# Kernel optimization log

Measured on AMD Instinct MI355X. Metric: run time of the kernel, lower is better.

The kernel has to match this reference:

```python
import jax, jax.numpy as jnp
import numpy as np

N_HEADS = 16
D_K = 64
MAX_LEN = 5000


def setup_inputs() -> dict:
    key = jax.random.key(0)
    ks = jax.random.split(key, 6)
    B, L, D = 4, 1024, 1024
    s = 1.0 / np.sqrt(D).astype(np.float32)
    return {
        "x": jax.random.normal(ks[0], (B, L, D), jnp.float32),
        "W_q": jax.random.normal(ks[1], (D, D), jnp.float32) * s,
        "b_q": jnp.zeros((D,), jnp.float32),
        "W_k": jax.random.normal(ks[2], (D, D), jnp.float32) * s,
        "b_k": jnp.zeros((D,), jnp.float32),
        "W_v": jax.random.normal(ks[3], (D, D), jnp.float32) * s,
        "b_v": jnp.zeros((D,), jnp.float32),
        "W_o": jax.random.normal(ks[4], (D, D), jnp.float32) * s,
        "b_o": jnp.zeros((D,), jnp.float32),
        "Er": jax.random.normal(ks[5], (MAX_LEN, D_K), jnp.float32) * 0.02,
    }


def reference(x, W_q, b_q, W_k, b_k, W_v, b_v, W_o, b_o, Er):
    B, L, D = x.shape
    H = N_HEADS
    dk = D // H
    # torch nn.Linear: y = x @ W.T + b
    Q = (x @ W_q.T + b_q).reshape(B, L, H, dk).transpose(0, 2, 1, 3)  # (B,H,L,dk)
    K = (x @ W_k.T + b_k).reshape(B, L, H, dk).transpose(0, 2, 1, 3)
    V = (x @ W_v.T + b_v).reshape(B, L, H, dk).transpose(0, 2, 1, 3)
    AC = jnp.einsum('bhid,bhjd->bhij', Q, K)  # (B,H,L,L)
    rel_pos = jnp.arange(L - 1, -L, -1) + (MAX_LEN - 1)  # (2L-1,)
    # mode='clip' matches intended math: clamped rows fall in the part that
    # the relative shift slices away.
    Er_embed = jnp.take(Er, rel_pos, axis=0, mode='clip')  # (2L-1, dk)
    BD = jnp.einsum('bhid,rd->bhir', Q, Er_embed)  # (B,H,L,2L-1)
    # _relative_shift: view is a no-op (shape already (B,H,L,2L-1)), then slice
    BD = BD[..., L - 1:]  # (B,H,L,L)
    scores = (AC + BD) / np.sqrt(dk).astype(np.float32)
    attn = jax.nn.softmax(scores, axis=-1)
    out = jnp.einsum('bhij,bhjd->bhid', attn, V)
    out = out.transpose(0, 2, 1, 3).reshape(B, L, D)
    return out @ W_o.T + b_o
```

## Files before the change

kernel.cpp:

```cpp
#include <hip/hip_runtime.h>
#include <cstdint>
#include <cstddef>


typedef __attribute__((ext_vector_type(8))) short short8;
typedef __attribute__((ext_vector_type(4))) float f32x4;

#define MFMA_BF16(a, b, c) __builtin_amdgcn_mfma_f32_16x16x32_bf16((a), (b), (c), 0, 0, 0)

constexpr int kB = 4, kL = 1024, kD = 1024, kH = 16;
constexpr int kBL = kB * kL;
constexpr float kScale = 0.125f * 1.44269504088896340736f;

static __device__ __forceinline__ unsigned short f32_to_bf16(float f) {
  union { float f; uint32_t u; } c; c.f = f;
  uint32_t u = c.u + 0x7fffu + ((c.u >> 16) & 1u);
  return (unsigned short)(u >> 16);
}

static __device__ __forceinline__ uint32_t pack_bf16x2(float a, float b) {
  union { float f; uint32_t u; } ca, cb; ca.f = a; cb.f = b;
  return ((ca.u + 0x8000u) >> 16) | ((cb.u + 0x8000u) & 0xffff0000u);
}

static __device__ __forceinline__ void gload_lds16(const void* g, void* l) {
  __builtin_amdgcn_global_load_lds(
      (const __attribute__((address_space(1))) void*)g,
      (__attribute__((address_space(3))) void*)l, 16, 0, 0);
}

__global__ __launch_bounds__(256)
void cast_all(const float* __restrict__ x,  const float* __restrict__ Wq,
              const float* __restrict__ Wk, const float* __restrict__ Wv,
              const float* __restrict__ Wo,
              unsigned short* __restrict__ xb, unsigned short* __restrict__ Wcat,
              unsigned short* __restrict__ Wob) {
  int i = blockIdx.x * blockDim.x + threadIdx.x;
  const float* src;
  ushort4* dst;
  int off;
  if (i < 1048576) {
    src = x; dst = reinterpret_cast<ushort4*>(xb); off = i;
  } else {
    int j = i - 1048576;
    int seg = j >> 18;
    off = j & 262143;
    if (seg == 0)      { src = Wq; dst = reinterpret_cast<ushort4*>(Wcat); }
    else if (seg == 1) { src = Wk; dst = reinterpret_cast<ushort4*>(Wcat) + 262144; }
    else if (seg == 2) { src = Wv; dst = reinterpret_cast<ushort4*>(Wcat) + 524288; }
    else               { src = Wo; dst = reinterpret_cast<ushort4*>(Wob); }
  }
  float4 v = reinterpret_cast<const float4*>(src)[off];
  ushort4 o;
  o.x = f32_to_bf16(v.x); o.y = f32_to_bf16(v.y);
  o.z = f32_to_bf16(v.z); o.w = f32_to_bf16(v.w);
  dst[off] = o;
}

__global__ __launch_bounds__(512, 2)
void gemm_qkv(const unsigned short* __restrict__ A,
              const unsigned short* __restrict__ Bm,
              const float* __restrict__ bq, const float* __restrict__ bk,
              const float* __restrict__ bv,
              const float* __restrict__ Er,
              unsigned short* __restrict__ Qh, unsigned short* __restrict__ Kh,
              unsigned short* __restrict__ Vth) {
  __shared__ __align__(16) char smem[114688];
  const int tid  = threadIdx.x;
  const int lane = tid & 63, wave = tid >> 6;
  const int quad = lane >> 4, l15 = lane & 15;
  const int wr = wave >> 2, wc = wave & 3;

  const int bid = blockIdx.x;
  const int xcd = bid & 7, idx = bid >> 3;
  const int m0 = ((xcd >> 1) * 4 + (idx >> 3)) * 256;
  const int n0 = ((xcd & 1) * 8 + (idx & 7)) * 192;

  const int aoff = (l15 >> 1) * 128 + (l15 & 1) * 64 +
                   ((quad * 16) ^ (((l15 >> 1) & 3) << 4)) + wr * 8192;
  const int b_lane = (quad * 16) ^ ((l15 & 7) << 4);
  const int boff = (wc * 48 + l15) * 128 + b_lane;

  int srowA[2], scolA[2];
#pragma unroll
  for (int j = 0; j < 2; ++j) {
    int poff = (j * 512 + tid) * 16;
    int L = poff ^ (((poff >> 7) & 3) << 4);
    srowA[j] = ((L >> 7) << 1) | ((L >> 6) & 1);
    scolA[j] = (L & 63) >> 1;
  }
  int srowB[3], scolB[3];
#pragma unroll
  for (int j = 0; j < 3; ++j) {
    int poff = (j * 512 + tid) * 16;
    int L = poff ^ (((poff >> 7) & 7) << 4);
    srowB[j] = L >> 7;
    scolB[j] = (L & 127) >> 1;
  }

  auto stageA = [&](int kh, int tt) {
    char* dst = smem + (tt & 1) * 32768 + kh * 16384 + tid * 16;
    const int kc = tt * 64 + kh * 32;
#pragma unroll
    for (int j = 0; j < 2; ++j)
      gload_lds16(A + (size_t)(m0 + srowA[j]) * 1024 + kc + scolA[j],
                  dst + j * 8192);
  };
  auto stageB = [&](int tt) {
    char* dst = smem + 65536 + (tt & 1) * 24576 + tid * 16;
    const int kc = tt * 64;
#pragma unroll
    for (int j = 0; j < 3; ++j)
      gload_lds16(Bm + (size_t)(n0 + srowB[j]) * 1024 + kc + scolB[j],
                  dst + j * 8192);
  };

  const f32x4 vzero = {0.f, 0.f, 0.f, 0.f};
  f32x4 acc[8][3];
#pragma unroll
  for (int i = 0; i < 8; ++i)
#pragma unroll
    for (int j = 0; j < 3; ++j) acc[i][j] = vzero;

  stageA(0, 0); stageB(0); stageA(1, 0); stageA(0, 1);
  asm volatile("s_waitcnt vmcnt(4)" ::: "memory");
  __builtin_amdgcn_s_barrier();

#define LDA(KH, MB) do {                                                      \
    _Pragma("unroll")                                                         \
    for (int f_ = 0; f_ < 4; ++f_)                                            \
      af[f_] = *(const short8*)(RA + (KH) * 16384 + aoff + ((MB) + f_) * 1024); \
  } while (0)
#define LDB(KH) do {                                                          \
    _Pragma("unroll")                                                         \
    for (int n_ = 0; n_ < 3; ++n_)                                            \
      bf[n_] = *(const short8*)(RB + ((boff + n_ * 2048) ^ ((KH) * 64)));     \
  } while (0)
#define BARA() do {                                                           \
    __builtin_amdgcn_s_barrier();                                             \
    asm volatile("s_waitcnt lgkmcnt(0)" ::: "memory");                        \
    __builtin_amdgcn_sched_barrier(0);                                        \
  } while (0)
#define MFMA_12(MB) do {                                                      \
    __builtin_amdgcn_s_setprio(1);                                            \
    _Pragma("unroll")                                                         \
    for (int mq_ = 0; mq_ < 4; ++mq_) {                                       \
      _Pragma("unroll")                                                       \
      for (int nq_ = 0; nq_ < 3; ++nq_)                                       \
        acc[(MB) + mq_][nq_] =                                                \
            MFMA_BF16(af[mq_], bf[nq_], acc[(MB) + mq_][nq_]);                \
    }                                                                         \
    __builtin_amdgcn_s_setprio(0);                                            \
  } while (0)

  for (int t = 0; t < 16; ++t) {
    const char* RA = smem + (t & 1) * 32768;
    const char* RB = smem + 65536 + (t & 1) * 24576;
    short8 af[4], bf[3];
    LDA(0, 0); LDB(0);
    if (t + 1 < 16) stageB(t + 1);
    BARA(); MFMA_12(0);
    __builtin_amdgcn_s_barrier();
    LDA(0, 4);
    if (t + 1 < 16) stageA(1, t + 1);
    BARA(); MFMA_12(4);
    if (t < 15) asm volatile("s_waitcnt vmcnt(7)" ::: "memory");
    else        asm volatile("s_waitcnt vmcnt(0)" ::: "memory");
    __builtin_amdgcn_s_barrier();
    LDA(1, 0); LDB(1);
    if (t + 2 < 16) stageA(0, t + 2);
    BARA(); MFMA_12(0);
    __builtin_amdgcn_s_barrier();
    LDA(1, 4);
    BARA(); MFMA_12(4);
    if (t < 14)       asm volatile("s_waitcnt vmcnt(4)" ::: "memory");
    else if (t == 14) asm volatile("s_waitcnt vmcnt(2)" ::: "memory");
    else              asm volatile("s_waitcnt vmcnt(0)" ::: "memory");
    __builtin_amdgcn_s_barrier();
  }

#undef LDA
#undef LDB
#undef BARA
#undef MFMA_12

  __syncthreads();
  const int gmb = m0 + wr * 128;
  const int bb  = gmb >> 10, i0l = gmb & 1023;
  unsigned short* Wv = (unsigned short*)smem + (size_t)wave * 6144;

#pragma unroll
  for (int nf = 0; nf < 3; ++nf) {
    const int n    = n0 + wc * 48 + nf * 16;
    const int wsel = n >> 10;
    const int nin  = n & 1023;
    const int hh   = nin >> 6, d0 = nin & 63;
    const size_t bh = (size_t)(bb * 16 + hh);

    if (wsel == 0) {
#pragma unroll
      for (int mf = 0; mf < 8; ++mf)
#pragma unroll
        for (int r = 0; r < 4; ++r) {
          const int i = i0l + mf * 16 + quad * 4 + r;
          float v = (acc[mf][nf][r] + bq[nin + l15]) * kScale;
          Qh[(bh * 1024 + i) * 64 + d0 + l15] = f32_to_bf16(v);
        }
    } else if (wsel == 1) {
#pragma unroll
      for (int mf = 0; mf < 8; ++mf)
#pragma unroll
        for (int r = 0; r < 4; ++r) {
          const int i = i0l + mf * 16 + quad * 4 + r;
          float v = acc[mf][nf][r] + bk[nin + l15] +
                    Er[(size_t)(4999 - i) * 64 + d0 + l15];
          Kh[(bh * 1024 + i) * 64 + d0 + l15] = f32_to_bf16(v);
        }
    } else {
      unsigned short* Wn = Wv + nf * 2048;
#pragma unroll
      for (int mf = 0; mf < 8; ++mf) {
        ushort4 pk;
        pk.x = f32_to_bf16(acc[mf][nf][0] + bv[nin + l15]);
        pk.y = f32_to_bf16(acc[mf][nf][1] + bv[nin + l15]);
        pk.z = f32_to_bf16(acc[mf][nf][2] + bv[nin + l15]);
        pk.w = f32_to_bf16(acc[mf][nf][3] + bv[nin + l15]);
        *(ushort4*)&Wn[(size_t)l15 * 128 + mf * 16 + quad * 4] = pk;
      }
#pragma unroll
      for (int p = 0; p < 4; ++p) {
        const int u = p * 64 + lane;
        const int dl = u >> 4, ch = (u & 15) * 8;
        short8 vv = *(const short8*)&Wn[(size_t)dl * 128 + ch];
        *(short8*)&Vth[(bh * 64 + d0 + dl) * 1024 + i0l + ch] = vv;
      }
    }
  }
}

__global__ __launch_bounds__(256)
void gemm_out(const unsigned short* __restrict__ A,
              const unsigned short* __restrict__ Bm,
              const float* __restrict__ bias,
              float* __restrict__ outf) {
  __shared__ __align__(16) char smem[49152];
  const int tid  = threadIdx.x;
  const int lane = tid & 63, wave = tid >> 6;
  const int quad = lane >> 4, l15 = lane & 15;
  const int m0 = blockIdx.y * 128, n0 = blockIdx.x * 64;

  const int afo = (l15 >> 1) * 128 + (l15 & 1) * 64 +
                  ((quad * 16) ^ (((l15 >> 1) & 3) << 4));

  int arow[4], acol[4], akh[4];
#pragma unroll
  for (int j = 0; j < 4; ++j) {
    int u = j * 256 + tid;
    akh[j] = u >> 9;
    int poff = (u & 511) * 16;
    int L = poff ^ (((poff >> 7) & 3) << 4);
    arow[j] = ((L >> 7) << 1) | ((L >> 6) & 1);
    acol[j] = (L & 63) >> 1;
  }
  int brow[2], bcol[2], bkh[2];
#pragma unroll
  for (int j = 0; j < 2; ++j) {
    int u = j * 256 + tid;
    bkh[j] = u >> 8;
    int poff = (u & 255) * 16;
    int L = poff ^ (((poff >> 7) & 3) << 4);
    brow[j] = ((L >> 7) << 1) | ((L >> 6) & 1);
    bcol[j] = (L & 63) >> 1;
  }

  auto stageG = [&](int buf, int t) {
    char* base = smem + buf * 24576;
    const int kc = t * 64;
#pragma unroll
    for (int j = 0; j < 4; ++j) {
      int u = j * 256 + tid;
      gload_lds16(A + (size_t)(m0 + arow[j]) * 1024 + kc + akh[j] * 32 + acol[j],
                  base + u * 16);
    }
#pragma unroll
    for (int j = 0; j < 2; ++j) {
      int u = j * 256 + tid;
      gload_lds16(Bm + (size_t)(n0 + brow[j]) * 1024 + kc + bkh[j] * 32 + bcol[j],
                  base + 16384 + u * 16);
    }
  };

  const f32x4 vzero = {0.f, 0.f, 0.f, 0.f};
  f32x4 acc[2][4];
#pragma unroll
  for (int i = 0; i < 2; ++i)
#pragma unroll
    for (int j = 0; j < 4; ++j) acc[i][j] = vzero;

  stageG(0, 0);
  for (int t = 0; t < 16; ++t) {
    const int cur = t & 1;
    if (t < 15) stageG(cur ^ 1, t + 1);
    if (t < 15) asm volatile("s_waitcnt vmcnt(6)" ::: "memory");
    else        asm volatile("s_waitcnt vmcnt(0)" ::: "memory");
    __builtin_amdgcn_s_barrier();
    __builtin_amdgcn_sched_barrier(0);
    const char* Ab = smem + cur * 24576;
    const char* Bb = Ab + 16384;
#pragma unroll
    for (int ks = 0; ks < 2; ++ks) {
      short8 af[2], bfv[4];
#pragma unroll
      for (int mt = 0; mt < 2; ++mt)
        af[mt] = *(const short8*)(Ab + ks * 8192 + wave * 2048 + mt * 1024 + afo);
#pragma unroll
      for (int nt = 0; nt < 4; ++nt)
        bfv[nt] = *(const short8*)(Bb + ks * 4096 + nt * 1024 + afo);
#pragma unroll
      for (int mt = 0; mt < 2; ++mt)
#pragma unroll
        for (int nt = 0; nt < 4; ++nt)
          acc[mt][nt] = MFMA_BF16(af[mt], bfv[nt], acc[mt][nt]);
    }
    __builtin_amdgcn_s_barrier();
    __builtin_amdgcn_sched_barrier(0);
  }

#pragma unroll
  for (int mt = 0; mt < 2; ++mt)
#pragma unroll
    for (int nt = 0; nt < 4; ++nt)
#pragma unroll
      for (int r = 0; r < 4; ++r) {
        const int gm = m0 + wave * 32 + mt * 16 + quad * 4 + r;
        const int gn = n0 + nt * 16 + l15;
        outf[(size_t)gm * 1024 + gn] = acc[mt][nt][r] + bias[gn];
      }
}

__global__ __launch_bounds__(256)
void attn_kernel(const unsigned short* __restrict__ Q,
                 const unsigned short* __restrict__ Kp,
                 const unsigned short* __restrict__ Vt,
                 unsigned short* __restrict__ Ao) {
  __shared__ unsigned short Ks[2][2][64 * 32];
  __shared__ unsigned short Vs[2][2][64 * 32];
  __shared__ unsigned short Plds[4][32 * 72];
  const int tid  = threadIdx.x;
  const int lane = tid & 63, wave = tid >> 6;
  const int quad = lane >> 4, l15 = lane & 15;
  const int bh = blockIdx.x;
  const int qb = blockIdx.y;
  const size_t base  = (size_t)bh * (kL * 64);
  const size_t vbase = (size_t)bh * (64 * kL);
  const int i0 = qb * 128 + wave * 32;

  short8 qf[2][2];
#pragma unroll
  for (int mt = 0; mt < 2; ++mt)
#pragma unroll
    for (int ks = 0; ks < 2; ++ks)
      qf[mt][ks] = *(const short8*)
          &Q[base + (size_t)(i0 + mt * 16 + l15) * 64 + ks * 32 + quad * 8];

  auto stage = [&](int buf, int kb) {
#pragma unroll
    for (int j = 0; j < 2; ++j) {
      int u = j * 256 + tid;
      int half = u >> 8, row = (u >> 2) & 63, c = (u & 3) * 8;
      gload_lds16(Kp + base + (size_t)(kb * 64 + row) * 64 + half * 32 + c,
                  (char*)&Ks[buf][0][0] + (size_t)u * 16);
      gload_lds16(Vt + vbase + (size_t)row * kL + kb * 64 + half * 32 + c,
                  (char*)&Vs[buf][0][0] + (size_t)u * 16);
    }
  };

  const f32x4 vzero = {0.f, 0.f, 0.f, 0.f};
  f32x4 of[2][4];
#pragma unroll
  for (int mt = 0; mt < 2; ++mt)
#pragma unroll
    for (int dt = 0; dt < 4; ++dt) of[mt][dt] = vzero;
  float lsum[2] = {0.f, 0.f};

  unsigned short* Pw = Plds[wave];

  stage(0, 0);
  __syncthreads();

  for (int kb = 0; kb < 16; ++kb) {
    const int cur = kb & 1, nxt = cur ^ 1;
    if (kb < 15) stage(nxt, kb + 1);

    short8 kf[4][2];
#pragma unroll
    for (int nt = 0; nt < 4; ++nt)
#pragma unroll
      for (int ks = 0; ks < 2; ++ks)
        kf[nt][ks] = *(const short8*)&Ks[cur][ks][(nt * 16 + l15) * 32 + quad * 8];
    f32x4 sf[2][4];
#pragma unroll
    for (int mt = 0; mt < 2; ++mt)
#pragma unroll
      for (int nt = 0; nt < 4; ++nt) {
        sf[mt][nt] = MFMA_BF16(kf[nt][0], qf[mt][0], vzero);
        sf[mt][nt] = MFMA_BF16(kf[nt][1], qf[mt][1], sf[mt][nt]);
      }

#pragma unroll
    for (int mt = 0; mt < 2; ++mt)
#pragma unroll
      for (int nt = 0; nt < 4; ++nt) {
        float p0 = __builtin_amdgcn_exp2f(sf[mt][nt][0]);
        float p1 = __builtin_amdgcn_exp2f(sf[mt][nt][1]);
        float p2 = __builtin_amdgcn_exp2f(sf[mt][nt][2]);
        float p3 = __builtin_amdgcn_exp2f(sf[mt][nt][3]);
        lsum[mt] += (p0 + p1) + (p2 + p3);
        uint2 w;
        w.x = pack_bf16x2(p0, p1);
        w.y = pack_bf16x2(p2, p3);
        *(uint2*)&Pw[(mt * 16 + l15) * 72 + nt * 16 + quad * 4] = w;
      }
    short8 pf[2][2];
#pragma unroll
    for (int mt = 0; mt < 2; ++mt)
#pragma unroll
      for (int ks = 0; ks < 2; ++ks)
        pf[mt][ks] = *(const short8*)&Pw[(mt * 16 + l15) * 72 + ks * 32 + quad * 8];

    short8 vf[4][2];
#pragma unroll
    for (int dt = 0; dt < 4; ++dt)
#pragma unroll
      for (int ks = 0; ks < 2; ++ks)
        vf[dt][ks] = *(const short8*)&Vs[cur][ks][(dt * 16 + l15) * 32 + quad * 8];
#pragma unroll
    for (int mt = 0; mt < 2; ++mt)
#pragma unroll
      for (int dt = 0; dt < 4; ++dt) {
        of[mt][dt] = MFMA_BF16(pf[mt][0], vf[dt][0], of[mt][dt]);
        of[mt][dt] = MFMA_BF16(pf[mt][1], vf[dt][1], of[mt][dt]);
      }

    __syncthreads();
  }

  float rl[2][4];
#pragma unroll
  for (int mt = 0; mt < 2; ++mt) {
    float s = lsum[mt];
    s += __shfl_xor(s, 16);
    s += __shfl_xor(s, 32);
#pragma unroll
    for (int r = 0; r < 4; ++r)
      rl[mt][r] = __builtin_amdgcn_rcpf(__shfl(s, quad * 4 + r));
  }

  const int b = bh >> 4, h = bh & 15;
#pragma unroll
  for (int mt = 0; mt < 2; ++mt)
#pragma unroll
    for (int dt = 0; dt < 4; ++dt)
#pragma unroll
      for (int r = 0; r < 4; ++r) {
        const int ig = i0 + mt * 16 + quad * 4 + r;
        float v = of[mt][dt][r] * rl[mt][r];
        Ao[((size_t)(b * 1024 + ig)) * 1024 + h * 64 + dt * 16 + l15] = f32_to_bf16(v);
      }
}

extern "C" void kernel_launch(void* const* d_in, const int* in_sizes, int n_in,
                              void* d_out, int out_size, void* d_ws, size_t ws_size,
                              hipStream_t stream) {
  const float* x   = (const float*)d_in[0];
  const float* W_q = (const float*)d_in[1];
  const float* b_q = (const float*)d_in[2];
  const float* W_k = (const float*)d_in[3];
  const float* b_k = (const float*)d_in[4];
  const float* W_v = (const float*)d_in[5];
  const float* b_v = (const float*)d_in[6];
  const float* W_o = (const float*)d_in[7];
  const float* b_o = (const float*)d_in[8];
  const float* Er  = (const float*)d_in[9];
  float* out = (float*)d_out;

  char* ws = (char*)d_ws;
  unsigned short* xb   = (unsigned short*)(ws + (size_t)0);
  unsigned short* Wcat = (unsigned short*)(ws + ((size_t)8  << 20));
  unsigned short* Wob  = (unsigned short*)(ws + ((size_t)14 << 20));
  unsigned short* Qh   = (unsigned short*)(ws + ((size_t)16 << 20));
  unsigned short* Kh   = (unsigned short*)(ws + ((size_t)24 << 20));
  unsigned short* Vth  = (unsigned short*)(ws + ((size_t)32 << 20));
  unsigned short* Aoh  = (unsigned short*)(ws + ((size_t)40 << 20));

  cast_all<<<8192, 256, 0, stream>>>(x, W_q, W_k, W_v, W_o, xb, Wcat, Wob);

  gemm_qkv<<<256, 512, 0, stream>>>(
      xb, Wcat, b_q, b_k, b_v, Er, Qh, Kh, Vth);

  attn_kernel<<<dim3(kB * kH, kL / 128), 256, 0, stream>>>(Qh, Kh, Vth, Aoh);

  gemm_out<<<dim3(16, 32), 256, 0, stream>>>(Aoh, Wob, b_o, out);
}
```

Before: 172.1 us.

## Retile QKV GEMM to 128x192 blocks with 4 waves and split-K staging

The QKV projection GEMM moves from 256x192 tiles with 8 waves per block to 128x192 tiles with 4 waves, launching twice as many blocks. Each wave now computes a 64x96 sub-tile, and the B operand is staged in two K halves using the same swizzle as A. This cuts LDS use per block and doubles grid size, which may raise occupancy and CU coverage. The cost is less operand reuse per block, so more global and LDS traffic per FLOP, plus an epilogue V-transpose buffer that reuses LDS without a preceding __syncthreads.

Result: no change. 172.9 us (+0.5%).

```diff
diff --git a/kernel.cpp b/kernel.cpp
--- a/kernel.cpp
+++ b/kernel.cpp
@@ -57,7 +57,7 @@
   dst[off] = o;
 }
 
-__global__ __launch_bounds__(512, 2)
+__global__ __launch_bounds__(256, 2)
 void gemm_qkv(const unsigned short* __restrict__ A,
               const unsigned short* __restrict__ Bm,
               const float* __restrict__ bq, const float* __restrict__ bk,
@@ -65,26 +65,25 @@
               const float* __restrict__ Er,
               unsigned short* __restrict__ Qh, unsigned short* __restrict__ Kh,
               unsigned short* __restrict__ Vth) {
-  __shared__ __align__(16) char smem[114688];
+  __shared__ __align__(16) char smem[81920];
   const int tid  = threadIdx.x;
   const int lane = tid & 63, wave = tid >> 6;
-  const int quad = lane >> 4, l15 = lane & 15;
-  const int wr = wave >> 2, wc = wave & 3;
+  const int quad = lane >> 4, l15 = lane & 15, lhalf = l15 >> 1;
+  const int wr = wave >> 1, wc = wave & 1;
 
   const int bid = blockIdx.x;
   const int xcd = bid & 7, idx = bid >> 3;
-  const int m0 = ((xcd >> 1) * 4 + (idx >> 3)) * 256;
+  const int m0 = ((xcd >> 1) * 8 + (idx >> 3)) * 128;
   const int n0 = ((xcd & 1) * 8 + (idx & 7)) * 192;
 
-  const int aoff = (l15 >> 1) * 128 + (l15 & 1) * 64 +
-                   ((quad * 16) ^ (((l15 >> 1) & 3) << 4)) + wr * 8192;
-  const int b_lane = (quad * 16) ^ ((l15 & 7) << 4);
-  const int boff = (wc * 48 + l15) * 128 + b_lane;
+  const int lane_off = (l15 & 1) * 64 + ((quad * 16) ^ ((lhalf & 3) << 4));
+  const int aoff = lhalf * 128 + lane_off + wr * 4096;
+  const int boff = lhalf * 128 + lane_off + wc * 6144;
 
   int srowA[2], scolA[2];
 #pragma unroll
   for (int j = 0; j < 2; ++j) {
-    int poff = (j * 512 + tid) * 16;
+    int poff = (j * 256 + tid) * 16;
     int L = poff ^ (((poff >> 7) & 3) << 4);
     srowA[j] = ((L >> 7) << 1) | ((L >> 6) & 1);
     scolA[j] = (L & 63) >> 1;
@@ -92,106 +91,96 @@
   int srowB[3], scolB[3];
 #pragma unroll
   for (int j = 0; j < 3; ++j) {
-    int poff = (j * 512 + tid) * 16;
-    int L = poff ^ (((poff >> 7) & 7) << 4);
-    srowB[j] = L >> 7;
-    scolB[j] = (L & 127) >> 1;
+    int poff = (j * 256 + tid) * 16;
+    int L = poff ^ (((poff >> 7) & 3) << 4);
+    srowB[j] = ((L >> 7) << 1) | ((L >> 6) & 1);
+    scolB[j] = (L & 63) >> 1;
   }
 
   auto stageA = [&](int kh, int tt) {
-    char* dst = smem + (tt & 1) * 32768 + kh * 16384 + tid * 16;
+    char* dst = smem + (tt & 1) * 16384 + kh * 8192 + tid * 16;
     const int kc = tt * 64 + kh * 32;
 #pragma unroll
     for (int j = 0; j < 2; ++j)
       gload_lds16(A + (size_t)(m0 + srowA[j]) * 1024 + kc + scolA[j],
-                  dst + j * 8192);
+                  dst + j * 4096);
   };
-  auto stageB = [&](int tt) {
-    char* dst = smem + 65536 + (tt & 1) * 24576 + tid * 16;
-    const int kc = tt * 64;
+  auto stageB = [&](int kh, int tt) {
+    char* dst = smem + 32768 + (tt & 1) * 24576 + kh * 12288 + tid * 16;
+    const int kc = tt * 64 + kh * 32;
 #pragma unroll
     for (int j = 0; j < 3; ++j)
       gload_lds16(Bm + (size_t)(n0 + srowB[j]) * 1024 + kc + scolB[j],
-                  dst + j * 8192);
+                  dst + j * 4096);
   };
 
   const f32x4 vzero = {0.f, 0.f, 0.f, 0.f};
-  f32x4 acc[8][3];
-#pragma unroll
-  for (int i = 0; i < 8; ++i)
-#pragma unroll
-    for (int j = 0; j < 3; ++j) acc[i][j] = vzero;
-
-  stageA(0, 0); stageB(0); stageA(1, 0); stageA(0, 1);
-  asm volatile("s_waitcnt vmcnt(4)" ::: "memory");
+  f32x4 acc[4][6];
+#pragma unroll
+  for (int i = 0; i < 4; ++i)
+#pragma unroll
+    for (int j = 0; j < 6; ++j) acc[i][j] = vzero;
+
+  stageA(0, 0); stageB(0, 0);
+  stageA(1, 0); stageB(1, 0);
+  stageA(0, 1); stageB(0, 1);
+  asm volatile("s_waitcnt vmcnt(10)" ::: "memory");
   __builtin_amdgcn_s_barrier();
 
-#define LDA(KH, MB) do {                                                      \
+#define LDAB(KH) do {                                                         \
     _Pragma("unroll")                                                         \
     for (int f_ = 0; f_ < 4; ++f_)                                            \
-      af[f_] = *(const short8*)(RA + (KH) * 16384 + aoff + ((MB) + f_) * 1024); \
-  } while (0)
-#define LDB(KH) do {                                                          \
+      af[f_] = *(const short8*)(RA + (KH) * 8192 + aoff + f_ * 1024);         \
     _Pragma("unroll")                                                         \
-    for (int n_ = 0; n_ < 3; ++n_)                                            \
-      bf[n_] = *(const short8*)(RB + ((boff + n_ * 2048) ^ ((KH) * 64)));     \
+    for (int n_ = 0; n_ < 6; ++n_)                                            \
+      bf[n_] = *(const short8*)(RB + (KH) * 12288 + boff + n_ * 1024);        \
   } while (0)
 #define BARA() do {                                                           \
     __builtin_amdgcn_s_barrier();                                             \
     asm volatile("s_waitcnt lgkmcnt(0)" ::: "memory");                        \
     __builtin_amdgcn_sched_barrier(0);                                        \
   } while (0)
-#define MFMA_12(MB) do {                                                      \
+#define MFMA_24() do {                                                        \
     __builtin_amdgcn_s_setprio(1);                                            \
     _Pragma("unroll")                                                         \
     for (int mq_ = 0; mq_ < 4; ++mq_) {                                       \
       _Pragma("unroll")                                                       \
-      for (int nq_ = 0; nq_ < 3; ++nq_)                                       \
-        acc[(MB) + mq_][nq_] =                                                \
-            MFMA_BF16(af[mq_], bf[nq_], acc[(MB) + mq_][nq_]);                \
+      for (int nq_ = 0; nq_ < 6; ++nq_)                                       \
+        acc[mq_][nq_] = MFMA_BF16(af[mq_], bf[nq_], acc[mq_][nq_]);           \
     }                                                                         \
     __builtin_amdgcn_s_setprio(0);                                            \
   } while (0)
 
   for (int t = 0; t < 16; ++t) {
-    const char* RA = smem + (t & 1) * 32768;
-    const char* RB = smem + 65536 + (t & 1) * 24576;
-    short8 af[4], bf[3];
-    LDA(0, 0); LDB(0);
-    if (t + 1 < 16) stageB(t + 1);
-    BARA(); MFMA_12(0);
-    __builtin_amdgcn_s_barrier();
-    LDA(0, 4);
-    if (t + 1 < 16) stageA(1, t + 1);
-    BARA(); MFMA_12(4);
-    if (t < 15) asm volatile("s_waitcnt vmcnt(7)" ::: "memory");
+    const char* RA = smem + (t & 1) * 16384;
+    const char* RB = smem + 32768 + (t & 1) * 24576;
+    short8 af[4], bf[6];
+    LDAB(0);
+    if (t + 1 < 16) { stageA(1, t + 1); stageB(1, t + 1); }
+    BARA(); MFMA_24();
+    if (t < 15) asm volatile("s_waitcnt vmcnt(10)" ::: "memory");
     else        asm volatile("s_waitcnt vmcnt(0)" ::: "memory");
     __builtin_amdgcn_s_barrier();
-    LDA(1, 0); LDB(1);
-    if (t + 2 < 16) stageA(0, t + 2);
-    BARA(); MFMA_12(0);
-    __builtin_amdgcn_s_barrier();
-    LDA(1, 4);
-    BARA(); MFMA_12(4);
-    if (t < 14)       asm volatile("s_waitcnt vmcnt(4)" ::: "memory");
-    else if (t == 14) asm volatile("s_waitcnt vmcnt(2)" ::: "memory");
+    LDAB(1);
+    if (t + 2 < 16) { stageA(0, t + 2); stageB(0, t + 2); }
+    BARA(); MFMA_24();
+    if (t < 14)       asm volatile("s_waitcnt vmcnt(10)" ::: "memory");
+    else if (t == 14) asm volatile("s_waitcnt vmcnt(5)" ::: "memory");
     else              asm volatile("s_waitcnt vmcnt(0)" ::: "memory");
     __builtin_amdgcn_s_barrier();
   }
 
-#undef LDA
-#undef LDB
+#undef LDAB
 #undef BARA
-#undef MFMA_12
-
-  __syncthreads();
-  const int gmb = m0 + wr * 128;
+#undef MFMA_24
+
+  const int gmb = m0 + wr * 64;
   const int bb  = gmb >> 10, i0l = gmb & 1023;
-  unsigned short* Wv = (unsigned short*)smem + (size_t)wave * 6144;
-
-#pragma unroll
-  for (int nf = 0; nf < 3; ++nf) {
-    const int n    = n0 + wc * 48 + nf * 16;
+  unsigned short* Wv = (unsigned short*)smem + (size_t)wave * 2048;
+
+#pragma unroll
+  for (int nf = 0; nf < 6; ++nf) {
+    const int n    = n0 + wc * 96 + nf * 16;
     const int wsel = n >> 10;
     const int nin  = n & 1023;
     const int hh   = nin >> 6, d0 = nin & 63;
@@ -199,7 +188,7 @@
 
     if (wsel == 0) {
 #pragma unroll
-      for (int mf = 0; mf < 8; ++mf)
+      for (int mf = 0; mf < 4; ++mf)
 #pragma unroll
         for (int r = 0; r < 4; ++r) {
           const int i = i0l + mf * 16 + quad * 4 + r;
@@ -208,7 +197,7 @@
         }
     } else if (wsel == 1) {
 #pragma unroll
-      for (int mf = 0; mf < 8; ++mf)
+      for (int mf = 0; mf < 4; ++mf)
 #pragma unroll
         for (int r = 0; r < 4; ++r) {
           const int i = i0l + mf * 16 + quad * 4 + r;
@@ -217,21 +206,20 @@
           Kh[(bh * 1024 + i) * 64 + d0 + l15] = f32_to_bf16(v);
         }
     } else {
-      unsigned short* Wn = Wv + nf * 2048;
-#pragma unroll
-      for (int mf = 0; mf < 8; ++mf) {
+#pragma unroll
+      for (int mf = 0; mf < 4; ++mf) {
         ushort4 pk;
         pk.x = f32_to_bf16(acc[mf][nf][0] + bv[nin + l15]);
         pk.y = f32_to_bf16(acc[mf][nf][1] + bv[nin + l15]);
         pk.z = f32_to_bf16(acc[mf][nf][2] + bv[nin + l15]);
         pk.w = f32_to_bf16(acc[mf][nf][3] + bv[nin + l15]);
-        *(ushort4*)&Wn[(size_t)l15 * 128 + mf * 16 + quad * 4] = pk;
-      }
-#pragma unroll
-      for (int p = 0; p < 4; ++p) {
+        *(ushort4*)&Wv[(size_t)l15 * 64 + mf * 16 + quad * 4] = pk;
+      }
+#pragma unroll
+      for (int p = 0; p < 2; ++p) {
         const int u = p * 64 + lane;
-        const int dl = u >> 4, ch = (u & 15) * 8;
-        short8 vv = *(const short8*)&Wn[(size_t)dl * 128 + ch];
+        const int dl = u >> 3, ch = (u & 7) * 8;
+        short8 vv = *(const short8*)&Wv[(size_t)dl * 64 + ch];
         *(short8*)&Vth[(bh * 64 + d0 + dl) * 1024 + i0l + ch] = vv;
       }
     }
@@ -495,7 +483,7 @@
 
   cast_all<<<8192, 256, 0, stream>>>(x, W_q, W_k, W_v, W_o, xb, Wcat, Wob);
 
-  gemm_qkv<<<256, 512, 0, stream>>>(
+  gemm_qkv<<<512, 256, 0, stream>>>(
       xb, Wcat, b_q, b_k, b_v, Er, Qh, Kh, Vth);
 
   attn_kernel<<<dim3(kB * kH, kL / 128), 256, 0, stream>>>(Qh, Kh, Vth, Aoh);
```
